# Optimization experiments

Hardware: AMD Instinct MI355X
Metric: run time of the kernel (lower is better)

The kernel has to match this reference:

```python
import jax, jax.numpy as jnp
import numpy as np

B, T, I, H, O = 256, 128, 64, 2048, 24


def setup_inputs() -> dict:
    key = jax.random.key(0)
    ks = jax.random.split(key, 10)
    sI = 1.0 / np.sqrt(I)
    sH = 1.0 / np.sqrt(H)
    return {
        "trains": jax.random.normal(ks[0], (B, T, I), jnp.float32),
        "dec": jax.random.normal(ks[1], (B, O - 1), jnp.float32),
        # packed gate projections, order [i, f, o, c] along last dim
        "Wx": jax.random.normal(ks[2], (I, 4 * H), jnp.float32) * sI,
        "bx": jax.random.normal(ks[3], (4 * H,), jnp.float32) * sI,
        "Wh": jax.random.normal(ks[4], (H, 4 * H), jnp.float32) * sH,
        "bh": jax.random.normal(ks[5], (4 * H,), jnp.float32) * sH,
        "Win": jax.random.normal(ks[6], (1, I), jnp.float32),
        "b_in": jax.random.normal(ks[7], (I,), jnp.float32),
        "Wout": jax.random.normal(ks[8], (H, 1), jnp.float32) * sH,
        "bout": jax.random.normal(ks[9], (1,), jnp.float32) * sH,
    }


def reference(trains, dec, Wx, bx, Wh, bh, Win, b_in, Wout, bout):
    def cell(h, c, x):
        # fused gate GEMMs: x@Wx and h@Wh each produce all 4 gates at once
        g = x @ Wx + bx + h @ Wh + bh  # [B, 4H]
        i, f, o, cc = jnp.split(g, 4, axis=-1)
        c = jax.nn.sigmoid(f) * c + jax.nn.sigmoid(i) * jnp.tanh(cc)
        h = jax.nn.sigmoid(o) * jnp.tanh(c)
        return h, c

    b = trains.shape[0]
    hdim = Wh.shape[0]
    h0 = jnp.zeros((b, hdim), trains.dtype)
    c0 = jnp.zeros((b, hdim), trains.dtype)

    def enc_step(carry, x):
        h, c = cell(*carry, x)
        return (h, c), None

    (h, c), _ = jax.lax.scan(enc_step, (h0, c0), jnp.swapaxes(trains, 0, 1))
    y1 = h @ Wout + bout  # [B, 1]

    def dec_step(carry, x_scalar):
        x = x_scalar[:, None] @ Win + b_in  # [B, I]
        h, c = cell(*carry, x)
        return (h, c), h @ Wout + bout  # emit [B, 1]

    (h, c), ys = jax.lax.scan(dec_step, (h, c), dec.T)  # ys: [O-1, B, 1]
    return jnp.concatenate([y1, jnp.swapaxes(ys[..., 0], 0, 1)], axis=1)  # [B, O]
```

## Files before the change

### kernel.cpp

```cpp
#include <hip/hip_runtime.h>


#define NB 256
#define NH 2048
#define NI 64
#define NK 2112
#define NPK 8192
#define NSTEPS 151
#define NO 24

typedef __bf16 bf16x8 __attribute__((ext_vector_type(8)));
typedef short short8 __attribute__((ext_vector_type(8)));
typedef short s16x4 __attribute__((ext_vector_type(4)));
typedef float f32x4 __attribute__((ext_vector_type(4)));
typedef unsigned short u16;

__device__ __forceinline__ u16 f2bf(float f) {
  union { float f; unsigned u; } v; v.f = f;
  unsigned r = v.u + 0x7FFFu + ((v.u >> 16) & 1u);
  return (u16)(r >> 16);
}

__device__ __forceinline__ void gload16(const void* g, void* l) {
  __builtin_amdgcn_global_load_lds(
      (const __attribute__((address_space(1))) unsigned int*)g,
      (__attribute__((address_space(3))) unsigned int*)l, 16, 0, 0);
}

__device__ __forceinline__ float sigmoidf_(float x) { return 1.f / (1.f + __expf(-x)); }
__device__ __forceinline__ float tanhf_(float x) {
  x = fminf(15.f, fmaxf(-15.f, x));
  float e = __expf(2.f * x);
  return (e - 1.f) / (e + 1.f);
}

__global__ __launch_bounds__(256) void wl_pack_w(const float* __restrict__ Wx,
                                                 const float* __restrict__ Wh,
                                                 u16* __restrict__ Wp) {
  __shared__ float s[64][65];
  const int j0 = blockIdx.x * 64, k0 = blockIdx.y * 64;
  const int tid = threadIdx.x;
  const int jl = tid & 63, kg = tid >> 6;
#pragma unroll
  for (int it = 0; it < 16; ++it) {
    int kl = it * 4 + kg;
    int k = k0 + kl, j = j0 + jl;
    float v = (k < NH) ? Wh[(size_t)k * NPK + j] : Wx[(size_t)(k - NH) * NPK + j];
    s[kl][jl] = v;
  }
  __syncthreads();
  int j = j0 + jl;
  int p = (j & (NH - 1)) * 4 + (j >> 11);
  short8 v0, v1;
#pragma unroll
  for (int e = 0; e < 8; ++e) {
    v0[e] = (short)f2bf(s[kg * 16 + e][jl]);
    v1[e] = (short)f2bf(s[kg * 16 + 8 + e][jl]);
  }
  short8* dst = (short8*)(Wp + (size_t)p * NK + k0 + kg * 16);
  dst[0] = v0;
  dst[1] = v1;
}

__global__ __launch_bounds__(256) void wl_bsum(const float* __restrict__ bx,
                                               const float* __restrict__ bh,
                                               float* __restrict__ bsum) {
  int p = blockIdx.x * 256 + threadIdx.x;
  int j = (p & 3) * NH + (p >> 2);
  bsum[p] = bx[j] + bh[j];
}

__global__ __launch_bounds__(256) void wl_xall(const float* __restrict__ trains,
                                               const float* __restrict__ dec,
                                               const float* __restrict__ Win,
                                               const float* __restrict__ b_in,
                                               u16* __restrict__ xall) {
  int idx = blockIdx.x * 256 + threadIdx.x;
  int i = idx & 63;
  int b = (idx >> 6) & 255;
  int t = idx >> 14;
  float v;
  if (t < 128) v = trains[((size_t)b * 128 + t) * 64 + i];
  else         v = dec[b * 23 + (t - 128)] * Win[i] + b_in[i];
  xall[idx] = f2bf(v);
}

__global__ __launch_bounds__(512) void wl_step(const u16* __restrict__ Wpg,
                                               const float* __restrict__ bsum,
                                               const u16* __restrict__ xall,
                                               u16* __restrict__ hcat,
                                               float* __restrict__ c_t,
                                               float* __restrict__ ypart,
                                               const float* __restrict__ Wout,
                                               int t) {
  __shared__ char arena[147456];

  const int bid = blockIdx.x;
  const int cs = (bid & 7) * 16 + ((bid >> 3) & 15);
  const int rh = bid >> 7;
  const int p0 = cs * 64, u0 = cs * 16, b0 = rh * 128;

  const int tid = threadIdx.x;
  const int wv = tid >> 6, lane = tid & 63;
  const int l15 = lane & 15, lhi = lane >> 4;
  const int srow = lane >> 3, sc = lane & 7;
  const int g8 = sc ^ srow;

  const u16* __restrict__ hin = hcat + (size_t)(t & 1) * NB * NH;
  u16* __restrict__ hout = hcat + (size_t)((t + 1) & 1) * NB * NH;

  f32x4 acc[4] = {};

  auto stage = [&](int kt, int buf) {
    char* const base = arena + buf * 24576;
    const u16* asrc; size_t astr;
    if (kt < 32) { asrc = hin + (size_t)b0 * NH + (size_t)kt * 64; astr = NH; }
    else         { asrc = xall + ((size_t)t * NB + b0) * NI;       astr = NI; }
#pragma unroll
    for (int i = 0; i < 2; ++i) {
      int qa = wv * 2 + i;
      int row = qa * 8 + srow;
      gload16(asrc + (size_t)row * astr + g8 * 8, base + qa * 1024);
    }
    const u16* bsrc = Wpg + (size_t)p0 * NK + (size_t)kt * 64;
    {
      int col = wv * 8 + srow;
      gload16(bsrc + (size_t)col * NK + g8 * 8, base + 16384 + wv * 1024);
    }
  };

  auto compute = [&](int kt, int buf) {
    const char* Ab = arena + buf * 24576;
    const char* Bb = Ab + 16384;
#pragma unroll
    for (int kc = 0; kc < 2; ++kc) {
      const int c8 = kc * 4 + lhi;
      bf16x8 bfr[4];
#pragma unroll
      for (int n = 0; n < 4; ++n) {
        int col = n * 16 + l15;
        bfr[n] = *(const bf16x8*)(Bb + col * 128 + ((c8 ^ (col & 7)) << 4));
      }
      int row = wv * 16 + l15;
      bf16x8 afr = *(const bf16x8*)(Ab + row * 128 + ((c8 ^ (row & 7)) << 4));
#pragma unroll
      for (int n = 0; n < 4; ++n)
        acc[n] = __builtin_amdgcn_mfma_f32_16x16x32_bf16(afr, bfr[n], acc[n], 0, 0, 0);
    }
  };

  stage(0, 0); stage(1, 1); stage(2, 2); stage(3, 3); stage(4, 4);
  int buf = 0;
  for (int kt = 0; kt < 33; ++kt) {
    if (kt < 29)       asm volatile("s_waitcnt vmcnt(12)" ::: "memory");
    else if (kt == 29) asm volatile("s_waitcnt vmcnt(9)" ::: "memory");
    else if (kt == 30) asm volatile("s_waitcnt vmcnt(6)" ::: "memory");
    else if (kt == 31) asm volatile("s_waitcnt vmcnt(3)" ::: "memory");
    else               asm volatile("s_waitcnt vmcnt(0)" ::: "memory");
    asm volatile("s_barrier" ::: "memory");
    if (kt <= 27) {
      int sb = buf + 5; if (sb >= 6) sb -= 6;
      stage(kt + 5, sb);
    }
    compute(kt, buf);
    if (++buf == 6) buf = 0;
  }

  __syncthreads();
#pragma unroll
  for (int n = 0; n < 4; ++n) {
    int col = n * 16 + l15;
    int chunk = wv * 4 + lhi;
    *(f32x4*)(arena + col * 512 + ((chunk ^ (col & 7)) << 4)) = acc[n];
  }
  __syncthreads();

  {
    const int bl = tid & 127, ug = tid >> 7;
    const int bg = b0 + bl;
    const bool emit = (t >= 127);
    float yacc = 0.f;
    s16x4 hv;
#pragma unroll
    for (int j = 0; j < 4; ++j) {
      int ul = ug * 4 + j;
      float g[4];
#pragma unroll
      for (int gi = 0; gi < 4; ++gi) {
        int col = ul * 4 + gi;
        g[gi] = *(const float*)(arena + col * 512 +
                                (((bl >> 2) ^ (col & 7)) << 4) + (bl & 3) * 4);
      }
      const float4 bs = *(const float4*)(bsum + p0 + ul * 4);
      float si = sigmoidf_(g[0] + bs.x);
      float sf = sigmoidf_(g[1] + bs.y);
      float so = sigmoidf_(g[2] + bs.z);
      float tc = tanhf_(g[3] + bs.w);
      size_t ci = (size_t)(u0 + ul) * NB + bg;
      float cn = sf * c_t[ci] + si * tc;
      float h = so * tanhf_(cn);
      c_t[ci] = cn;
      hv[j] = (short)f2bf(h);
      if (emit) yacc += h * Wout[u0 + ul];
    }
    *(s16x4*)(hout + (size_t)bg * NH + u0 + ug * 4) = hv;
    if (emit) ypart[((size_t)(t - 127) * 512 + cs * 4 + ug) * NB + bg] = yacc;
  }
}

__global__ __launch_bounds__(256) void wl_finy(const float* __restrict__ ypart,
                                               const float* __restrict__ bout,
                                               float* __restrict__ out) {
  int j = blockIdx.x;
  int b = threadIdx.x;
  const float* yp = ypart + (size_t)j * 512 * NB;
  float s = bout[0];
#pragma unroll 8
  for (int i = 0; i < 512; ++i) s += yp[i * NB + b];
  out[b * NO + j] = s;
}

extern "C" void kernel_launch(void* const* d_in, const int* in_sizes, int n_in,
                              void* d_out, int out_size, void* d_ws, size_t ws_size,
                              hipStream_t stream) {
  const float* trains = (const float*)d_in[0];
  const float* dec    = (const float*)d_in[1];
  const float* Wx     = (const float*)d_in[2];
  const float* bx     = (const float*)d_in[3];
  const float* Wh     = (const float*)d_in[4];
  const float* bh     = (const float*)d_in[5];
  const float* Win    = (const float*)d_in[6];
  const float* b_in   = (const float*)d_in[7];
  const float* Wout   = (const float*)d_in[8];
  const float* bout   = (const float*)d_in[9];
  float* out = (float*)d_out;
  char* ws = (char*)d_ws;

  u16*   Wp    = (u16*)(ws);
  float* bsum  = (float*)(ws + 34603008);
  u16*   xall  = (u16*)(ws + 34635776);
  u16*   hcat  = (u16*)(ws + 39583744);
  float* c_t   = (float*)(ws + 41680896);
  float* ypart = (float*)(ws + 43778048);

  (void)hipMemsetAsync(ws + 39583744, 0, 4194304, stream);
  wl_pack_w<<<dim3(128, 33), 256, 0, stream>>>(Wx, Wh, Wp);
  wl_bsum<<<32, 256, 0, stream>>>(bx, bh, bsum);
  wl_xall<<<(NSTEPS * NB * NI) / 256, 256, 0, stream>>>(trains, dec, Win, b_in, xall);
  for (int t = 0; t < NSTEPS; ++t)
    wl_step<<<256, 512, 0, stream>>>(Wp, bsum, xall, hcat, c_t, ypart, Wout, t);
  wl_finy<<<NO, 256, 0, stream>>>(ypart, bout, out);
}
```

Before: 2.961 ms.

## Use 32x32x16 MFMA with 2-wave blocks and larger per-wave tiles

The step kernel now runs 2 waves per block instead of 8. Each wave computes a 64x64 output tile with four 32x32x16 bf16 MFMAs per k-slice, replacing one 16x64 strip built from 16x16 MFMAs. LDS staging and the epilogue layout are reworked so each thread handles one batch row and all 16 hidden units, which cuts the y-partial count from 512 to 128. The aim is more MFMA work per LDS fragment load and less reduction traffic, at the cost of fewer waves to hide global-load latency and more global loads issued per thread.

```diff
diff --git a/kernel.cpp b/kernel.cpp
--- a/kernel.cpp
+++ b/kernel.cpp
@@ -11,8 +11,8 @@
 
 typedef __bf16 bf16x8 __attribute__((ext_vector_type(8)));
 typedef short short8 __attribute__((ext_vector_type(8)));
-typedef short s16x4 __attribute__((ext_vector_type(4)));
 typedef float f32x4 __attribute__((ext_vector_type(4)));
+typedef float f32x16 __attribute__((ext_vector_type(16)));
 typedef unsigned short u16;
 
 __device__ __forceinline__ u16 f2bf(float f) {
@@ -85,7 +85,7 @@
   xall[idx] = f2bf(v);
 }
 
-__global__ __launch_bounds__(512) void wl_step(const u16* __restrict__ Wpg,
+__global__ __launch_bounds__(128) void wl_step(const u16* __restrict__ Wpg,
                                                const float* __restrict__ bsum,
                                                const u16* __restrict__ xall,
                                                u16* __restrict__ hcat,
@@ -102,95 +102,93 @@
 
   const int tid = threadIdx.x;
   const int wv = tid >> 6, lane = tid & 63;
-  const int l15 = lane & 15, lhi = lane >> 4;
-  const int srow = lane >> 3, sc = lane & 7;
-  const int g8 = sc ^ srow;
+  const int l31 = lane & 31, lh = lane >> 5;
 
   const u16* __restrict__ hin = hcat + (size_t)(t & 1) * NB * NH;
   u16* __restrict__ hout = hcat + (size_t)((t + 1) & 1) * NB * NH;
 
-  f32x4 acc[4] = {};
+  f32x16 acc00 = {}, acc01 = {}, acc10 = {}, acc11 = {};
 
   auto stage = [&](int kt, int buf) {
     char* const base = arena + buf * 24576;
-    const u16* asrc; size_t astr;
-    if (kt < 32) { asrc = hin + (size_t)b0 * NH + (size_t)kt * 64; astr = NH; }
-    else         { asrc = xall + ((size_t)t * NB + b0) * NI;       astr = NI; }
-#pragma unroll
-    for (int i = 0; i < 2; ++i) {
-      int qa = wv * 2 + i;
-      int row = qa * 8 + srow;
-      gload16(asrc + (size_t)row * astr + g8 * 8, base + qa * 1024);
-    }
-    const u16* bsrc = Wpg + (size_t)p0 * NK + (size_t)kt * 64;
-    {
-      int col = wv * 8 + srow;
-      gload16(bsrc + (size_t)col * NK + g8 * 8, base + 16384 + wv * 1024);
+    const u16* asrc; int astr;
+    if (kt < 32) { asrc = hin + (size_t)b0 * NH + kt * 64; astr = NH; }
+    else         { asrc = xall + ((size_t)t * NB + b0) * NI; astr = NI; }
+#pragma unroll
+    for (int i = 0; i < 8; ++i) {
+      int j = wv * 8 + i;
+      int kc = j >> 1, r8 = j & 1;
+      int row = r8 * 64 + lane;
+      gload16(asrc + (size_t)row * astr + kc * 8, base + kc * 2048 + r8 * 1024);
+    }
+    const u16* bsrc = Wpg + (size_t)(p0 + lane) * NK + kt * 64;
+#pragma unroll
+    for (int i = 0; i < 4; ++i) {
+      int kc = wv * 4 + i;
+      gload16(bsrc + kc * 8, base + 16384 + kc * 1024);
     }
   };
 
-  auto compute = [&](int kt, int buf) {
+  auto compute = [&](int buf) {
     const char* Ab = arena + buf * 24576;
     const char* Bb = Ab + 16384;
 #pragma unroll
-    for (int kc = 0; kc < 2; ++kc) {
-      const int c8 = kc * 4 + lhi;
-      bf16x8 bfr[4];
-#pragma unroll
-      for (int n = 0; n < 4; ++n) {
-        int col = n * 16 + l15;
-        bfr[n] = *(const bf16x8*)(Bb + col * 128 + ((c8 ^ (col & 7)) << 4));
-      }
-      int row = wv * 16 + l15;
-      bf16x8 afr = *(const bf16x8*)(Ab + row * 128 + ((c8 ^ (row & 7)) << 4));
-#pragma unroll
-      for (int n = 0; n < 4; ++n)
-        acc[n] = __builtin_amdgcn_mfma_f32_16x16x32_bf16(afr, bfr[n], acc[n], 0, 0, 0);
+    for (int s = 0; s < 4; ++s) {
+      int kc = s * 2 + lh;
+      bf16x8 a0 = *(const bf16x8*)(Ab + kc * 2048 + (wv * 64 + l31) * 16);
+      bf16x8 a1 = *(const bf16x8*)(Ab + kc * 2048 + (wv * 64 + 32 + l31) * 16);
+      bf16x8 bf0 = *(const bf16x8*)(Bb + kc * 1024 + l31 * 16);
+      bf16x8 bf1 = *(const bf16x8*)(Bb + kc * 1024 + (32 + l31) * 16);
+      acc00 = __builtin_amdgcn_mfma_f32_32x32x16_bf16(a0, bf0, acc00, 0, 0, 0);
+      acc01 = __builtin_amdgcn_mfma_f32_32x32x16_bf16(a0, bf1, acc01, 0, 0, 0);
+      acc10 = __builtin_amdgcn_mfma_f32_32x32x16_bf16(a1, bf0, acc10, 0, 0, 0);
+      acc11 = __builtin_amdgcn_mfma_f32_32x32x16_bf16(a1, bf1, acc11, 0, 0, 0);
     }
   };
 
   stage(0, 0); stage(1, 1); stage(2, 2); stage(3, 3); stage(4, 4);
-  int buf = 0;
   for (int kt = 0; kt < 33; ++kt) {
-    if (kt < 29)       asm volatile("s_waitcnt vmcnt(12)" ::: "memory");
-    else if (kt == 29) asm volatile("s_waitcnt vmcnt(9)" ::: "memory");
-    else if (kt == 30) asm volatile("s_waitcnt vmcnt(6)" ::: "memory");
-    else if (kt == 31) asm volatile("s_waitcnt vmcnt(3)" ::: "memory");
+    if (kt <= 28)      asm volatile("s_waitcnt vmcnt(48)" ::: "memory");
+    else if (kt == 29) asm volatile("s_waitcnt vmcnt(36)" ::: "memory");
+    else if (kt == 30) asm volatile("s_waitcnt vmcnt(24)" ::: "memory");
+    else if (kt == 31) asm volatile("s_waitcnt vmcnt(12)" ::: "memory");
     else               asm volatile("s_waitcnt vmcnt(0)" ::: "memory");
     asm volatile("s_barrier" ::: "memory");
-    if (kt <= 27) {
-      int sb = buf + 5; if (sb >= 6) sb -= 6;
+    if (kt + 5 <= 32) {
+      int sb = kt + 5 - ((kt + 5 >= 6) ? 6 : 0); sb = (kt + 5) % 6;
       stage(kt + 5, sb);
     }
-    compute(kt, buf);
-    if (++buf == 6) buf = 0;
+    compute(kt % 6);
   }
 
   __syncthreads();
-#pragma unroll
-  for (int n = 0; n < 4; ++n) {
-    int col = n * 16 + l15;
-    int chunk = wv * 4 + lhi;
-    *(f32x4*)(arena + col * 512 + ((chunk ^ (col & 7)) << 4)) = acc[n];
+  {
+    char* gt = arena;
+#pragma unroll
+    for (int rb = 0; rb < 2; ++rb)
+#pragma unroll
+      for (int cb = 0; cb < 2; ++cb) {
+        const f32x16& a = rb ? (cb ? acc11 : acc10) : (cb ? acc01 : acc00);
+#pragma unroll
+        for (int r = 0; r < 16; ++r) {
+          int row = wv * 64 + rb * 32 + (r & 3) + 8 * (r >> 2) + 4 * lh;
+          int col = cb * 32 + l31;
+          *(float*)(gt + row * 256 + (((col >> 2) ^ (row & 15)) << 4) +
+                    (col & 3) * 4) = a[r];
+        }
+      }
   }
   __syncthreads();
 
   {
-    const int bl = tid & 127, ug = tid >> 7;
+    const int bl = tid;
     const int bg = b0 + bl;
     const bool emit = (t >= 127);
     float yacc = 0.f;
-    s16x4 hv;
-#pragma unroll
-    for (int j = 0; j < 4; ++j) {
-      int ul = ug * 4 + j;
-      float g[4];
-#pragma unroll
-      for (int gi = 0; gi < 4; ++gi) {
-        int col = ul * 4 + gi;
-        g[gi] = *(const float*)(arena + col * 512 +
-                                (((bl >> 2) ^ (col & 7)) << 4) + (bl & 3) * 4);
-      }
+    short8 hva, hvb;
+#pragma unroll
+    for (int ul = 0; ul < 16; ++ul) {
+      f32x4 g = *(const f32x4*)(arena + bl * 256 + ((ul ^ (bl & 15)) << 4));
       const float4 bs = *(const float4*)(bsum + p0 + ul * 4);
       float si = sigmoidf_(g[0] + bs.x);
       float sf = sigmoidf_(g[1] + bs.y);
@@ -200,11 +198,12 @@
       float cn = sf * c_t[ci] + si * tc;
       float h = so * tanhf_(cn);
       c_t[ci] = cn;
-      hv[j] = (short)f2bf(h);
+      if (ul < 8) hva[ul] = (short)f2bf(h); else hvb[ul - 8] = (short)f2bf(h);
       if (emit) yacc += h * Wout[u0 + ul];
     }
-    *(s16x4*)(hout + (size_t)bg * NH + u0 + ug * 4) = hv;
-    if (emit) ypart[((size_t)(t - 127) * 512 + cs * 4 + ug) * NB + bg] = yacc;
+    *(short8*)(hout + (size_t)bg * NH + u0) = hva;
+    *(short8*)(hout + (size_t)bg * NH + u0 + 8) = hvb;
+    if (emit) ypart[((size_t)(t - 127) * 128 + cs) * NB + bg] = yacc;
   }
 }
 
@@ -213,10 +212,10 @@
                                                float* __restrict__ out) {
   int j = blockIdx.x;
   int b = threadIdx.x;
-  const float* yp = ypart + (size_t)j * 512 * NB;
+  const float* yp = ypart + (size_t)j * 128 * NB;
   float s = bout[0];
 #pragma unroll 8
-  for (int i = 0; i < 512; ++i) s += yp[i * NB + b];
+  for (int i = 0; i < 128; ++i) s += yp[i * NB + b];
   out[b * NO + j] = s;
 }
 
@@ -240,14 +239,14 @@
   float* bsum  = (float*)(ws + 34603008);
   u16*   xall  = (u16*)(ws + 34635776);
   u16*   hcat  = (u16*)(ws + 39583744);
-  float* c_t   = (float*)(ws + 41680896);
-  float* ypart = (float*)(ws + 43778048);
-
-  (void)hipMemsetAsync(ws + 39583744, 0, 4194304, stream);
+  float* c_t   = (float*)(ws + 43778048);
+  float* ypart = (float*)(ws + 45875200);
+
+  (void)hipMemsetAsync(ws + 39583744, 0, 6291456, stream);
   wl_pack_w<<<dim3(128, 33), 256, 0, stream>>>(Wx, Wh, Wp);
   wl_bsum<<<32, 256, 0, stream>>>(bx, bh, bsum);
   wl_xall<<<(NSTEPS * NB * NI) / 256, 256, 0, stream>>>(trains, dec, Win, b_in, xall);
   for (int t = 0; t < NSTEPS; ++t)
-    wl_step<<<256, 512, 0, stream>>>(Wp, bsum, xall, hcat, c_t, ypart, Wout, t);
+    wl_step<<<256, 128, 0, stream>>>(Wp, bsum, xall, hcat, c_t, ypart, Wout, t);
   wl_finy<<<NO, 256, 0, stream>>>(ypart, bout, out);
 }
```

Measured after the change: 5.049 ms. 1.7x slower.
